# Kernel tuning notes

Measured on AMD Instinct MI355X. Metric: run time of the kernel, lower is better.

## Reference

```python
import jax, jax.numpy as jnp
import numpy as np

N_IN, M_MID = 512, 256
B, H, W = 16, 64, 64

def setup_inputs() -> dict:
    key = jax.random.key(0)
    ks = jax.random.split(key, 7)
    s = 0.05
    return {
        "x": jax.random.normal(ks[0], (B, N_IN, H, W), dtype=jnp.float32),
        "W_state": jax.random.normal(ks[1], (M_MID, N_IN), dtype=jnp.float32) * s,
        "b_state": jax.random.normal(ks[2], (M_MID,), dtype=jnp.float32) * s,
        "W_proj": jax.random.normal(ks[3], (M_MID, N_IN), dtype=jnp.float32) * s,
        "b_proj": jax.random.normal(ks[4], (M_MID,), dtype=jnp.float32) * s,
        "W_extend": jax.random.normal(ks[5], (N_IN, M_MID), dtype=jnp.float32) * s,
        "b_extend": jax.random.normal(ks[6], (N_IN,), dtype=jnp.float32) * s,
    }

def reference(x, W_state, b_state, W_proj, b_proj, W_extend, b_extend):
    n, c, h, w = x.shape
    hw = h * w
    xf = x.reshape(n, c, hw)                                   # [n, C, HW]
    # 1x1 convs are channel GEMMs over flattened spatial dim
    x_state = jnp.einsum('mc,nch->nmh', W_state, xf) + b_state[None, :, None]   # [n, M, HW]
    x_proj = jnp.einsum('mc,nch->nmh', W_proj, xf) + b_proj[None, :, None]      # [n, M, HW]
    # bmm -> scale -> softmax -> bmm (graph reasoning over M x M)
    scores = jnp.einsum('nmh,nkh->nmk', x_state, x_proj) / jnp.sqrt(jnp.float32(hw))
    attn = jax.nn.softmax(scores, axis=2)                      # [n, M, M]
    x_rstate = jnp.einsum('nmk,nkh->nmh', attn, x_proj)        # [n, M, HW]
    # extend back to C channels + residual
    ext = jnp.einsum('cm,nmh->nch', W_extend, x_rstate) + b_extend[None, :, None]
    return x + ext.reshape(n, c, h, w)
```

## Files before the change

### kernel.cpp

```cpp
#include <hip/hip_runtime.h>
#include <hip/hip_bf16.h>
#include <stdint.h>

typedef __bf16 bf16x8_t __attribute__((ext_vector_type(8)));
typedef float  f32x4_t  __attribute__((ext_vector_type(4)));
typedef short  short8_t __attribute__((ext_vector_type(8)));

__device__ __forceinline__ unsigned short f2b(float f) {
    union { float f; unsigned u; } v; v.f = f;
    unsigned u = v.u;
    return (unsigned short)((u + 0x7FFFu + ((u >> 16) & 1u)) >> 16);
}
__device__ __forceinline__ float b2f(unsigned short b) {
    union { unsigned u; float f; } v; v.u = ((unsigned)b) << 16; return v.f;
}

#define AS3(p) ((__attribute__((address_space(3))) void*)(p))
#define AS1(p) ((const __attribute__((address_space(1))) void*)(p))
#define FENCE() asm volatile("" ::: "memory")

#define NB   16
#define CIN  512
#define MMID 256
#define HW   4096
#define KSPLIT 4
#define ASZ  (128 * 64)
#define ASZA3 (256 * 64)
#define ASZB3 (64 * 64)

__device__ __forceinline__ void swz3(int gx, int gy, int& bx, int& by, int& bz) {
    const int nwg = gridDim.x, ord = blockIdx.x, q = nwg >> 3;
    const int s = (ord & 7) * q + (ord >> 3);
    by = s % gy;
    const int rem = s / gy;
    bx = rem % gx;
    bz = rem / gx;
}

__global__ __launch_bounds__(256) void prep_weights(
    const float* __restrict__ Ws, const float* __restrict__ Wp,
    const float* __restrict__ Wef, const float* __restrict__ bs,
    const float* __restrict__ bp,
    unsigned short* __restrict__ Wsp, unsigned short* __restrict__ Wex,
    unsigned short* __restrict__ WpT, float* __restrict__ bsp)
{
    int i = blockIdx.x * 256 + threadIdx.x;
    if (i < MMID * CIN) {
        Wsp[i]              = f2b(Ws[i]);
        Wsp[MMID * CIN + i] = f2b(Wp[i]);
        Wex[i]              = f2b(Wef[i]);
        const int c = i >> 8, k = i & (MMID - 1);
        WpT[i] = f2b(Wp[(size_t)k * CIN + c]);
    }
    if (i < MMID) { bsp[i] = bs[i]; bsp[MMID + i] = bp[i]; }
}

__global__ __launch_bounds__(256) void transpose_convert_x(
    const float* __restrict__ x, unsigned short* __restrict__ xT)
{
    __shared__ unsigned short tile[64][66];
    const int n = blockIdx.z, c0 = blockIdx.y * 64, h0 = blockIdx.x * 64;
    const float* s = x + ((size_t)n * CIN + c0) * HW + h0;
    unsigned short* d = xT + ((size_t)n * HW + h0) * CIN + c0;
    const int t = threadIdx.x;
    {
        const int rr = t >> 4, cc = (t & 15) * 4;
        #pragma unroll
        for (int p = 0; p < 4; ++p) {
            int r = p * 16 + rr;
            float4 v = *(const float4*)(s + (size_t)r * HW + cc);
            tile[r][cc + 0] = f2b(v.x); tile[r][cc + 1] = f2b(v.y);
            tile[r][cc + 2] = f2b(v.z); tile[r][cc + 3] = f2b(v.w);
        }
    }
    __syncthreads();
    {
        const int wr = t >> 3, wc = (t & 7) * 8;
        #pragma unroll
        for (int p = 0; p < 2; ++p) {
            int h = p * 32 + wr;
            unsigned short tmp[8];
            #pragma unroll
            for (int j = 0; j < 8; ++j) tmp[j] = tile[wc + j][h];
            *(short8_t*)(d + (size_t)h * CIN + wc) = *(const short8_t*)tmp;
        }
    }
}

__global__ __launch_bounds__(256) void transpose_bf16_64(
    const unsigned short* __restrict__ src, unsigned short* __restrict__ dst,
    int srs, int drs, long long sbs, long long dbs)
{
    __shared__ unsigned short tile[64][66];
    const int n = blockIdx.z, r0 = blockIdx.y * 64, c0 = blockIdx.x * 64;
    const unsigned short* s = src + (size_t)n * sbs + (size_t)r0 * srs + c0;
    unsigned short* d = dst + (size_t)n * dbs + (size_t)c0 * drs + r0;
    const int t = threadIdx.x;
    const int rr = t >> 3, cc = (t & 7) * 8;
    #pragma unroll
    for (int p = 0; p < 2; ++p) {
        int r = p * 32 + rr;
        short8_t v = *(const short8_t*)(s + (size_t)r * srs + cc);
        #pragma unroll
        for (int j = 0; j < 8; ++j) tile[r][cc + j] = ((const unsigned short*)&v)[j];
    }
    __syncthreads();
    #pragma unroll
    for (int p = 0; p < 2; ++p) {
        int c = p * 32 + rr;
        unsigned short tmp[8];
        #pragma unroll
        for (int j = 0; j < 8; ++j) tmp[j] = tile[cc + j][c];
        *(short8_t*)(d + (size_t)c * drs + cc) = *(const short8_t*)tmp;
    }
}

template <int EPI>
__device__ __forceinline__ void epilogue_repack(
    f32x4_t (&acc)[4][4], unsigned short* smem,
    int m0, int n0, int wave, int lane,
    void* __restrict__ Cout, int ldc, size_t cbase)
{
    float* fbuf = (float*)smem;
    const int t   = wave * 64 + lane;
    const int l15 = lane & 15, l16 = lane >> 4;
    const int wr2 = wave >> 1;
    const int wc  = (wave & 1) * 64;

    #pragma unroll
    for (int p = 0; p < 4; ++p) {
        __syncthreads();
        if (wr2 == (p >> 1)) {
            const int ihalf = p & 1;
            #pragma unroll
            for (int i2 = 0; i2 < 2; ++i2) {
                const int i = ihalf * 2 + i2;
                #pragma unroll
                for (int r = 0; r < 4; ++r) {
                    const int lrow = i2 * 16 + l16 * 4 + r;
                    #pragma unroll
                    for (int j = 0; j < 4; ++j)
                        fbuf[lrow * 132 + wc + j * 16 + l15] = acc[i][j][r];
                }
            }
        }
        __syncthreads();
        #pragma unroll
        for (int it = 0; it < 2; ++it) {
            const int lrow = it * 16 + (t >> 4);
            const int col  = (t & 15) * 8;
            const int row  = m0 + p * 32 + lrow;
            float v[8];
            *(float4*)&v[0] = *(const float4*)&fbuf[lrow * 132 + col];
            *(float4*)&v[4] = *(const float4*)&fbuf[lrow * 132 + col + 4];
            const size_t idx = cbase + (size_t)row * ldc + n0 + col;
            if constexpr (EPI == 1) {
                float* op = (float*)Cout + idx;
                *(float4*)op = *(const float4*)&v[0];
                *(float4*)(op + 4) = *(const float4*)&v[4];
            } else if constexpr (EPI == 4) {
                unsigned short o[8];
                #pragma unroll
                for (int k = 0; k < 8; ++k)
                    o[k] = f2b(v[k] + ((row == n0 + col + k) ? 1.0f : 0.0f));
                *(short8_t*)((unsigned short*)Cout + idx) = *(const short8_t*)o;
            } else {
                unsigned short o[8];
                #pragma unroll
                for (int k = 0; k < 8; ++k) o[k] = f2b(v[k]);
                *(short8_t*)((unsigned short*)Cout + idx) = *(const short8_t*)o;
            }
        }
    }
}

#define GEMM_KLOOP(Ab, Bb, lda, ldb, KBEG, NT)                                          \
    auto stage = [&](int k0, int b) {                                                   \
        unsigned short* Asb = smem + b * 2 * ASZ;                                       \
        unsigned short* Bsb = Asb + ASZ;                                                \
        _Pragma("unroll")                                                               \
        for (int c = 0; c < 4; ++c) {                                                   \
            const int o   = (c * 256 + t) * 16;                                         \
            const int row = o >> 7;                                                     \
            const int ce  = ((o & 127) ^ ((row & 7) << 4)) >> 1;                        \
            __builtin_amdgcn_global_load_lds(                                           \
                AS1(Ab + (size_t)row * lda + k0 + ce), AS3((char*)Asb + o), 16, 0, 0);  \
            __builtin_amdgcn_global_load_lds(                                           \
                AS1(Bb + (size_t)row * ldb + k0 + ce), AS3((char*)Bsb + o), 16, 0, 0);  \
        }                                                                               \
    };                                                                                  \
    stage(KBEG, 0);                                                                     \
    for (int itk = 0; itk < (NT); ++itk) {                                              \
        const int cur = itk & 1;                                                        \
        if (itk + 1 < (NT)) {                                                           \
            stage(KBEG + (itk + 1) * 64, cur ^ 1);                                      \
            asm volatile("s_waitcnt vmcnt(8)" ::: "memory");                            \
        } else {                                                                        \
            asm volatile("s_waitcnt vmcnt(0)" ::: "memory");                            \
        }                                                                               \
        __builtin_amdgcn_s_barrier();                                                   \
        FENCE();                                                                        \
        const char* Asb = (const char*)(smem + cur * 2 * ASZ);                          \
        const char* Bsb = Asb + 2 * ASZ;                                                \
        const int swz = (l15 & 7) << 4;                                                 \
        _Pragma("unroll")                                                               \
        for (int ks = 0; ks < 2; ++ks) {                                                \
            bf16x8_t af[4], bfr[4];                                                     \
            const int cb = (ks * 64 + l16 * 16) ^ swz;                                  \
            _Pragma("unroll")                                                           \
            for (int i = 0; i < 4; ++i) {                                               \
                af[i]  = *(const bf16x8_t*)(Asb + (wr + i * 16 + l15) * 128 + cb);      \
                bfr[i] = *(const bf16x8_t*)(Bsb + (wc + i * 16 + l15) * 128 + cb);      \
            }                                                                           \
            _Pragma("unroll")                                                           \
            for (int i = 0; i < 4; ++i)                                                 \
                _Pragma("unroll")                                                       \
                for (int j = 0; j < 4; ++j)                                             \
                    acc[i][j] = __builtin_amdgcn_mfma_f32_16x16x32_bf16(                \
                        af[i], bfr[j], acc[i][j], 0, 0, 0);                             \
        }                                                                               \
        FENCE();                                                                        \
        __builtin_amdgcn_s_barrier();                                                   \
        FENCE();                                                                        \
    }

template <int EPI>
__global__ __launch_bounds__(256, 2) void gemm_occ2(
    const unsigned short* __restrict__ A, const unsigned short* __restrict__ B,
    long long strideA, long long strideB,
    const float* __restrict__ bias, int bias_bstride,
    void* __restrict__ Cout, int ldc, long long strideC,
    int gx, int gy)
{
    __shared__ unsigned short smem[2 * (ASZA3 + ASZB3)];

    int bx, by, n;  swz3(gx, gy, bx, by, n);
    const int m0 = by * 256;
    const int n0 = bx * 64;

    const unsigned short* Ab = A + (size_t)n * strideA + (size_t)m0 * CIN;
    const unsigned short* Bb = B + (size_t)n * strideB + (size_t)n0 * CIN;

    const int t    = threadIdx.x;
    const int lane = t & 63;
    const int wave = t >> 6;
    const int wr   = wave * 64;
    const int l15  = lane & 15;
    const int l16  = lane >> 4;

    f32x4_t acc[4][4] = {};

    auto stage = [&](int k0, int b) {
        unsigned short* Asb = smem + b * (ASZA3 + ASZB3);
        unsigned short* Bsb = Asb + ASZA3;
        #pragma unroll
        for (int c = 0; c < 8; ++c) {
            const int o   = (c * 256 + t) * 16;
            const int row = o >> 7;
            const int ce  = ((o & 127) ^ ((row & 7) << 4)) >> 1;
            __builtin_amdgcn_global_load_lds(
                AS1(Ab + (size_t)row * CIN + k0 + ce), AS3((char*)Asb + o), 16, 0, 0);
        }
        #pragma unroll
        for (int c = 0; c < 2; ++c) {
            const int o   = (c * 256 + t) * 16;
            const int row = o >> 7;
            const int ce  = ((o & 127) ^ ((row & 7) << 4)) >> 1;
            __builtin_amdgcn_global_load_lds(
                AS1(Bb + (size_t)row * CIN + k0 + ce), AS3((char*)Bsb + o), 16, 0, 0);
        }
    };

    const int NT = CIN / 64;
    stage(0, 0);
    for (int itk = 0; itk < NT; ++itk) {
        const int cur = itk & 1;
        if (itk + 1 < NT) {
            stage((itk + 1) * 64, cur ^ 1);
            asm volatile("s_waitcnt vmcnt(10)" ::: "memory");
        } else {
            asm volatile("s_waitcnt vmcnt(0)" ::: "memory");
        }
        __builtin_amdgcn_s_barrier();
        FENCE();
        const char* Asb = (const char*)(smem + cur * (ASZA3 + ASZB3));
        const char* Bsb = Asb + 2 * ASZA3;
        const int swz = (l15 & 7) << 4;
        #pragma unroll
        for (int ks = 0; ks < 2; ++ks) {
            const int cb = (ks * 64 + l16 * 16) ^ swz;
            bf16x8_t af[4], bfr[4];
            #pragma unroll
            for (int i = 0; i < 4; ++i)
                af[i] = *(const bf16x8_t*)(Asb + (wr + i * 16 + l15) * 128 + cb);
            #pragma unroll
            for (int j = 0; j < 4; ++j)
                bfr[j] = *(const bf16x8_t*)(Bsb + (j * 16 + l15) * 128 + cb);
            #pragma unroll
            for (int i = 0; i < 4; ++i)
                #pragma unroll
                for (int j = 0; j < 4; ++j)
                    acc[i][j] = __builtin_amdgcn_mfma_f32_16x16x32_bf16(
                        af[i], bfr[j], acc[i][j], 0, 0, 0);
        }
        FENCE();
        __builtin_amdgcn_s_barrier();
        FENCE();
    }

    float* fbuf = (float*)smem;
    const size_t cbase = (size_t)n * strideC;
    const float* beff = bias + (size_t)n * bias_bstride;
    #pragma unroll
    for (int p = 0; p < 8; ++p) {
        __syncthreads();
        if (wave == (p >> 1)) {
            #pragma unroll
            for (int i2 = 0; i2 < 2; ++i2) {
                const int i = (p & 1) * 2 + i2;
                #pragma unroll
                for (int r = 0; r < 4; ++r) {
                    const int lrow = i2 * 16 + l16 * 4 + r;
                    #pragma unroll
                    for (int j = 0; j < 4; ++j)
                        fbuf[lrow * 68 + j * 16 + l15] = acc[i][j][r];
                }
            }
        }
        __syncthreads();
        const int lrow = t >> 3;
        const int col  = (t & 7) * 8;
        const int row  = m0 + p * 32 + lrow;
        float v[8];
        *(float4*)&v[0] = *(const float4*)&fbuf[lrow * 68 + col];
        *(float4*)&v[4] = *(const float4*)&fbuf[lrow * 68 + col + 4];
        const float badd = beff[row];
        const size_t idx = cbase + (size_t)row * ldc + n0 + col;
        if constexpr (EPI == 1) {
            float o[8];
            #pragma unroll
            for (int k = 0; k < 8; ++k) o[k] = v[k] + badd;
            float* op = (float*)Cout + idx;
            *(float4*)op = *(const float4*)&o[0];
            *(float4*)(op + 4) = *(const float4*)&o[4];
        } else {
            unsigned short o[8];
            #pragma unroll
            for (int k = 0; k < 8; ++k) o[k] = f2b(v[k] + badd);
            *(short8_t*)((unsigned short*)Cout + idx) = *(const short8_t*)o;
        }
    }
}

__global__ __launch_bounds__(256) void gemm_scores(
    const unsigned short* __restrict__ Ysp, float* __restrict__ scoresP)
{
    __shared__ unsigned short smem[4 * ASZ];

    int bx, by, z;  swz3(MMID / 128, MMID / 128, bx, by, z);
    const int n  = z >> 2;
    const int kc = z & 3;
    const int m0 = by * 128;
    const int n0 = bx * 128;

    const unsigned short* Ab = Ysp + (size_t)n * CIN * HW + (size_t)m0 * HW;
    const unsigned short* Bb = Ysp + (size_t)n * CIN * HW + (size_t)(MMID + n0) * HW;

    const int t    = threadIdx.x;
    const int lane = t & 63;
    const int wave = t >> 6;
    const int wr   = (wave >> 1) * 64;
    const int wc   = (wave & 1) * 64;
    const int l15  = lane & 15;
    const int l16  = lane >> 4;

    f32x4_t acc[4][4] = {};
    const int kbeg = kc * (HW / KSPLIT);
    GEMM_KLOOP(Ab, Bb, HW, HW, kbeg, (HW / KSPLIT) / 64)

    float* outp = scoresP + (size_t)(kc * NB + n) * MMID * MMID;
    epilogue_repack<1>(acc, smem, m0, n0, wave, lane, outp, MMID, 0);
}

__global__ __launch_bounds__(256) void softmax_rows(
    const float* __restrict__ scoresP, unsigned short* __restrict__ attn)
{
    const int wave = threadIdx.x >> 6;
    const int l    = threadIdx.x & 63;
    const size_t row = (size_t)blockIdx.x * 4 + wave;
    const size_t pstride = (size_t)NB * MMID * MMID;
    float4 v = {0.f, 0.f, 0.f, 0.f};
    #pragma unroll
    for (int p = 0; p < KSPLIT; ++p) {
        float4 u = *(const float4*)(scoresP + p * pstride + row * MMID + l * 4);
        v.x += u.x; v.y += u.y; v.z += u.z; v.w += u.w;
    }
    float mx = fmaxf(fmaxf(v.x, v.y), fmaxf(v.z, v.w));
    #pragma unroll
    for (int off = 32; off; off >>= 1) mx = fmaxf(mx, __shfl_xor(mx, off));
    const float sc = 0.015625f;
    float e0 = __expf((v.x - mx) * sc), e1 = __expf((v.y - mx) * sc);
    float e2 = __expf((v.z - mx) * sc), e3 = __expf((v.w - mx) * sc);
    float sum = e0 + e1 + e2 + e3;
    #pragma unroll
    for (int off = 32; off; off >>= 1) sum += __shfl_xor(sum, off);
    const float inv = 1.0f / sum;
    unsigned short o[4] = { f2b(e0 * inv), f2b(e1 * inv), f2b(e2 * inv), f2b(e3 * inv) };
    *(uint64_t*)(attn + row * MMID + l * 4) = *(const uint64_t*)o;
}

__global__ __launch_bounds__(256) void compute_vec(
    const unsigned short* __restrict__ G, const float* __restrict__ bsp,
    const float* __restrict__ be, float* __restrict__ vec)
{
    const int n = blockIdx.x >> 1;
    const int c = ((blockIdx.x & 1) << 8) + threadIdx.x;
    const unsigned short* g = G + ((size_t)n * CIN + c) * MMID;
    float s = 0.f;
    for (int k = 0; k < MMID; k += 8) {
        short8_t v = *(const short8_t*)(g + k);
        #pragma unroll
        for (int j = 0; j < 8; ++j)
            s += b2f((unsigned short)v[j]) * bsp[MMID + k + j];
    }
    vec[n * CIN + c] = be[c] + s;
}

template <int EPI>
__global__ __launch_bounds__(256) void gemm_nt(
    const unsigned short* __restrict__ A, const unsigned short* __restrict__ B,
    int lda, int ldb, int K,
    long long strideA, long long strideB,
    void* __restrict__ Cout, int ldc, long long strideC,
    int gx, int gy)
{
    __shared__ unsigned short smem[4 * ASZ];

    int bx, by, n;  swz3(gx, gy, bx, by, n);
    const int m0 = by * 128;
    const int n0 = bx * 128;

    const unsigned short* Ab = A + (size_t)n * strideA + (size_t)m0 * lda;
    const unsigned short* Bb = B + (size_t)n * strideB + (size_t)n0 * ldb;

    const int t    = threadIdx.x;
    const int lane = t & 63;
    const int wave = t >> 6;
    const int wr   = (wave >> 1) * 64;
    const int wc   = (wave & 1) * 64;
    const int l15  = lane & 15;
    const int l16  = lane >> 4;

    f32x4_t acc[4][4] = {};
    GEMM_KLOOP(Ab, Bb, lda, ldb, 0, K / 64)

    epilogue_repack<EPI>(acc, smem, m0, n0, wave, lane,
                         Cout, ldc, (size_t)n * strideC);
}

extern "C" void kernel_launch(void* const* d_in, const int* in_sizes, int n_in,
                              void* d_out, int out_size, void* d_ws, size_t ws_size,
                              hipStream_t stream)
{
    const float* x   = (const float*)d_in[0];
    const float* Ws  = (const float*)d_in[1];
    const float* bs  = (const float*)d_in[2];
    const float* Wp  = (const float*)d_in[3];
    const float* bp  = (const float*)d_in[4];
    const float* Wef = (const float*)d_in[5];
    const float* be  = (const float*)d_in[6];
    float* out = (float*)d_out;

    unsigned short* xT   = (unsigned short*)d_ws;
    unsigned short* Ysp  = xT   + (size_t)NB * HW * CIN;
    unsigned short* Wsp  = Ysp  + (size_t)NB * CIN * HW;
    unsigned short* Wex  = Wsp  + (size_t)CIN * CIN;
    unsigned short* WpT  = Wex  + (size_t)CIN * MMID;
    unsigned short* attn = WpT  + (size_t)CIN * MMID;
    unsigned short* attnT= attn + (size_t)NB * MMID * MMID;
    unsigned short* G    = attnT+ (size_t)NB * MMID * MMID;
    unsigned short* Meff = G    + (size_t)NB * CIN * MMID;
    float* scoresP = (float*)(Meff + (size_t)NB * CIN * CIN);
    float* bsp = scoresP + (size_t)KSPLIT * NB * MMID * MMID;
    float* vec = bsp + CIN;

    prep_weights<<<512, 256, 0, stream>>>(Ws, Wp, Wef, bs, bp, Wsp, Wex, WpT, bsp);

    transpose_convert_x<<<dim3(HW / 64, CIN / 64, NB), 256, 0, stream>>>(x, xT);

    gemm_occ2<0><<<(CIN / 256) * (HW / 64) * NB, 256, 0, stream>>>(
        Wsp, xT, 0LL, (long long)HW * CIN,
        bsp, 0, Ysp, HW, (long long)CIN * HW,
        HW / 64, CIN / 256);

    gemm_scores<<<(MMID / 128) * (MMID / 128) * NB * KSPLIT, 256, 0, stream>>>(
        Ysp, scoresP);

    softmax_rows<<<NB * MMID / 4, 256, 0, stream>>>(scoresP, attn);

    transpose_bf16_64<<<dim3(MMID / 64, MMID / 64, NB), 256, 0, stream>>>(
        attn, attnT, MMID, MMID, (long long)MMID * MMID, (long long)MMID * MMID);

    gemm_nt<2><<<(MMID / 128) * (CIN / 128) * NB, 256, 0, stream>>>(
        Wex, attnT, MMID, MMID, MMID,
        0LL, (long long)MMID * MMID,
        G, MMID, (long long)CIN * MMID,
        MMID / 128, CIN / 128);

    compute_vec<<<NB * 2, 256, 0, stream>>>(G, bsp, be, vec);

    gemm_nt<4><<<(CIN / 128) * (CIN / 128) * NB, 256, 0, stream>>>(
        G, WpT, MMID, MMID, MMID,
        (long long)CIN * MMID, 0LL,
        Meff, CIN, (long long)CIN * CIN,
        CIN / 128, CIN / 128);

    gemm_occ2<1><<<(CIN / 256) * (HW / 64) * NB, 256, 0, stream>>>(
        Meff, xT, (long long)CIN * CIN, (long long)HW * CIN,
        vec, CIN, out, HW, (long long)CIN * HW,
        HW / 64, CIN / 256);
}
```

Before: 197.4 us.

## Replace occupancy-2 GEMM with 256x256-tile 8-wave eight-phase pipelined GEMM

The two big channel GEMMs (Wsp·x and Meff·x) move from a 256x64 tile with 4 waves and 2 blocks per CU to a 256x256 tile with 8 waves and one block per CU. The K loop is split into half-K-tile phases that interleave LDS fragment reads, async global-to-LDS loads and MFMA bursts raised with s_setprio. The LDS layout also gets a new XOR swizzle. The aim is more operand reuse per loaded byte and better overlap of memory traffic with compute, at the cost of lower occupancy, higher register pressure (128 accumulator floats per lane) and a more rigid synchronisation schedule.

```diff
diff --git a/kernel.cpp b/kernel.cpp
--- a/kernel.cpp
+++ b/kernel.cpp
@@ -25,8 +25,7 @@
 #define HW   4096
 #define KSPLIT 4
 #define ASZ  (128 * 64)
-#define ASZA3 (256 * 64)
-#define ASZB3 (64 * 64)
+#define PH_BUFB 65536
 
 __device__ __forceinline__ void swz3(int gx, int gy, int& bx, int& by, int& bz) {
     const int nwg = gridDim.x, ord = blockIdx.x, q = nwg >> 3;
@@ -225,18 +224,18 @@
     }
 
 template <int EPI>
-__global__ __launch_bounds__(256, 2) void gemm_occ2(
+__global__ __launch_bounds__(512, 1) void gemm_8ph(
     const unsigned short* __restrict__ A, const unsigned short* __restrict__ B,
     long long strideA, long long strideB,
     const float* __restrict__ bias, int bias_bstride,
     void* __restrict__ Cout, int ldc, long long strideC,
     int gx, int gy)
 {
-    __shared__ unsigned short smem[2 * (ASZA3 + ASZB3)];
+    __shared__ __attribute__((aligned(16))) char smem[2 * PH_BUFB];
 
     int bx, by, n;  swz3(gx, gy, bx, by, n);
     const int m0 = by * 256;
-    const int n0 = bx * 64;
+    const int n0 = bx * 256;
 
     const unsigned short* Ab = A + (size_t)n * strideA + (size_t)m0 * CIN;
     const unsigned short* Bb = B + (size_t)n * strideB + (size_t)n0 * CIN;
@@ -244,69 +243,96 @@
     const int t    = threadIdx.x;
     const int lane = t & 63;
     const int wave = t >> 6;
-    const int wr   = wave * 64;
+    const int wr2  = wave >> 2;
+    const int wc4  = wave & 3;
     const int l15  = lane & 15;
     const int l16  = lane >> 4;
 
-    f32x4_t acc[4][4] = {};
-
-    auto stage = [&](int k0, int b) {
-        unsigned short* Asb = smem + b * (ASZA3 + ASZB3);
-        unsigned short* Bsb = Asb + ASZA3;
-        #pragma unroll
-        for (int c = 0; c < 8; ++c) {
-            const int o   = (c * 256 + t) * 16;
-            const int row = o >> 7;
-            const int ce  = ((o & 127) ^ ((row & 7) << 4)) >> 1;
+    auto stage_half = [&](const unsigned short* base, int kt, int kh, char* dst) {
+        #pragma unroll
+        for (int c = 0; c < 2; ++c) {
+            const int ci = c * 512 + t;
+            const int r  = ci >> 2;
+            const int ssrc = (ci & 3) ^ ((r >> 1) & 3);
             __builtin_amdgcn_global_load_lds(
-                AS1(Ab + (size_t)row * CIN + k0 + ce), AS3((char*)Asb + o), 16, 0, 0);
-        }
-        #pragma unroll
-        for (int c = 0; c < 2; ++c) {
-            const int o   = (c * 256 + t) * 16;
-            const int row = o >> 7;
-            const int ce  = ((o & 127) ^ ((row & 7) << 4)) >> 1;
-            __builtin_amdgcn_global_load_lds(
-                AS1(Bb + (size_t)row * CIN + k0 + ce), AS3((char*)Bsb + o), 16, 0, 0);
+                AS1(base + (size_t)r * CIN + kt * 64 + kh * 32 + ssrc * 8),
+                AS3(dst + ci * 16), 16, 0, 0);
         }
     };
 
-    const int NT = CIN / 64;
-    stage(0, 0);
-    for (int itk = 0; itk < NT; ++itk) {
-        const int cur = itk & 1;
-        if (itk + 1 < NT) {
-            stage((itk + 1) * 64, cur ^ 1);
-            asm volatile("s_waitcnt vmcnt(10)" ::: "memory");
-        } else {
-            asm volatile("s_waitcnt vmcnt(0)" ::: "memory");
-        }
-        __builtin_amdgcn_s_barrier();
-        FENCE();
-        const char* Asb = (const char*)(smem + cur * (ASZA3 + ASZB3));
-        const char* Bsb = Asb + 2 * ASZA3;
-        const int swz = (l15 & 7) << 4;
-        #pragma unroll
-        for (int ks = 0; ks < 2; ++ks) {
-            const int cb = (ks * 64 + l16 * 16) ^ swz;
-            bf16x8_t af[4], bfr[4];
-            #pragma unroll
-            for (int i = 0; i < 4; ++i)
-                af[i] = *(const bf16x8_t*)(Asb + (wr + i * 16 + l15) * 128 + cb);
-            #pragma unroll
-            for (int j = 0; j < 4; ++j)
-                bfr[j] = *(const bf16x8_t*)(Bsb + (j * 16 + l15) * 128 + cb);
-            #pragma unroll
-            for (int i = 0; i < 4; ++i)
-                #pragma unroll
-                for (int j = 0; j < 4; ++j)
-                    acc[i][j] = __builtin_amdgcn_mfma_f32_16x16x32_bf16(
-                        af[i], bfr[j], acc[i][j], 0, 0, 0);
-        }
-        FENCE();
-        __builtin_amdgcn_s_barrier();
-        FENCE();
-    }
+    f32x4_t acc[8][4] = {};
+    bf16x8_t af4[4], bfr4[4];
+
+    auto read_af = [&](int ibase, int ks, const char* buf) {
+        #pragma unroll
+        for (int i = 0; i < 4; ++i) {
+            const int row = wr2 * 128 + (ibase + i) * 16 + l15;
+            af4[i] = *(const bf16x8_t*)(buf + ks * 16384 + row * 64
+                         + ((l16 ^ ((row >> 1) & 3)) << 4));
+        }
+    };
+    auto read_bfr = [&](int ks, const char* buf) {
+        #pragma unroll
+        for (int j = 0; j < 4; ++j) {
+            const int row = wc4 * 64 + j * 16 + l15;
+            bfr4[j] = *(const bf16x8_t*)(buf + 32768 + ks * 16384 + row * 64
+                         + ((l16 ^ ((row >> 1) & 3)) << 4));
+        }
+    };
+
+    #define PH_SYNC() do { asm volatile("s_waitcnt vmcnt(8)" ::: "memory"); \
+        __builtin_amdgcn_s_barrier(); FENCE(); } while (0)
+    #define PH_END() do { FENCE(); __builtin_amdgcn_s_barrier(); FENCE(); } while (0)
+    #define MFMA16(IB) do { __builtin_amdgcn_s_setprio(1); \
+        _Pragma("unroll") for (int i = 0; i < 4; ++i) \
+            _Pragma("unroll") for (int j = 0; j < 4; ++j) \
+                acc[(IB) + i][j] = __builtin_amdgcn_mfma_f32_16x16x32_bf16( \
+                    af4[i], bfr4[j], acc[(IB) + i][j], 0, 0, 0); \
+        __builtin_amdgcn_s_setprio(0); } while (0)
+
+    char* buf0 = smem;
+    char* buf1 = smem + PH_BUFB;
+
+    stage_half(Ab, 0, 0, buf0 + 0);
+    stage_half(Bb, 0, 0, buf0 + 32768);
+    stage_half(Ab, 0, 1, buf0 + 16384);
+    stage_half(Bb, 0, 1, buf0 + 49152);
+    stage_half(Ab, 1, 0, buf1 + 0);
+    stage_half(Bb, 1, 0, buf1 + 32768);
+    asm volatile("s_waitcnt vmcnt(8)" ::: "memory");
+    __builtin_amdgcn_s_barrier();
+    FENCE();
+
+    for (int g = 0; g < 4; ++g) {
+        const int t2 = 2 * g + 2, t3 = 2 * g + 3;
+        read_af(0, 0, buf0); read_bfr(0, buf0);
+        stage_half(Ab, 2 * g + 1, 1, buf1 + 16384);
+        PH_SYNC(); MFMA16(0); PH_END();
+        read_af(4, 0, buf0);
+        stage_half(Bb, 2 * g + 1, 1, buf1 + 49152);
+        PH_SYNC(); MFMA16(4); PH_END();
+        read_af(0, 1, buf0); read_bfr(1, buf0);
+        if (t2 < 8) stage_half(Ab, t2, 0, buf0 + 0);
+        PH_SYNC(); MFMA16(0); PH_END();
+        read_af(4, 1, buf0);
+        if (t2 < 8) stage_half(Bb, t2, 0, buf0 + 32768);
+        PH_SYNC(); MFMA16(4); PH_END();
+        read_af(0, 0, buf1); read_bfr(0, buf1);
+        if (t2 < 8) stage_half(Ab, t2, 1, buf0 + 16384);
+        PH_SYNC(); MFMA16(0); PH_END();
+        read_af(4, 0, buf1);
+        if (t2 < 8) stage_half(Bb, t2, 1, buf0 + 49152);
+        PH_SYNC(); MFMA16(4); PH_END();
+        read_af(0, 1, buf1); read_bfr(1, buf1);
+        if (t3 < 8) stage_half(Ab, t3, 0, buf1 + 0);
+        PH_SYNC(); MFMA16(0); PH_END();
+        read_af(4, 1, buf1);
+        if (t3 < 8) stage_half(Bb, t3, 0, buf1 + 32768);
+        PH_SYNC(); MFMA16(4); PH_END();
+    }
+    #undef PH_SYNC
+    #undef PH_END
+    #undef MFMA16
 
     float* fbuf = (float*)smem;
     const size_t cbase = (size_t)n * strideC;
@@ -314,40 +340,43 @@
     #pragma unroll
     for (int p = 0; p < 8; ++p) {
         __syncthreads();
-        if (wave == (p >> 1)) {
+        if (wr2 == (p >> 2)) {
             #pragma unroll
             for (int i2 = 0; i2 < 2; ++i2) {
-                const int i = (p & 1) * 2 + i2;
+                const int i = (p & 3) * 2 + i2;
                 #pragma unroll
                 for (int r = 0; r < 4; ++r) {
                     const int lrow = i2 * 16 + l16 * 4 + r;
                     #pragma unroll
                     for (int j = 0; j < 4; ++j)
-                        fbuf[lrow * 68 + j * 16 + l15] = acc[i][j][r];
+                        fbuf[lrow * 264 + wc4 * 64 + j * 16 + l15] = acc[i][j][r];
                 }
             }
         }
         __syncthreads();
-        const int lrow = t >> 3;
-        const int col  = (t & 7) * 8;
-        const int row  = m0 + p * 32 + lrow;
-        float v[8];
-        *(float4*)&v[0] = *(const float4*)&fbuf[lrow * 68 + col];
-        *(float4*)&v[4] = *(const float4*)&fbuf[lrow * 68 + col + 4];
-        const float badd = beff[row];
-        const size_t idx = cbase + (size_t)row * ldc + n0 + col;
-        if constexpr (EPI == 1) {
-            float o[8];
-            #pragma unroll
-            for (int k = 0; k < 8; ++k) o[k] = v[k] + badd;
-            float* op = (float*)Cout + idx;
-            *(float4*)op = *(const float4*)&o[0];
-            *(float4*)(op + 4) = *(const float4*)&o[4];
-        } else {
-            unsigned short o[8];
-            #pragma unroll
-            for (int k = 0; k < 8; ++k) o[k] = f2b(v[k] + badd);
-            *(short8_t*)((unsigned short*)Cout + idx) = *(const short8_t*)o;
+        #pragma unroll
+        for (int it = 0; it < 2; ++it) {
+            const int lrow = it * 16 + (t >> 5);
+            const int col  = (t & 31) * 8;
+            const int row  = m0 + p * 32 + lrow;
+            float v[8];
+            *(float4*)&v[0] = *(const float4*)&fbuf[lrow * 264 + col];
+            *(float4*)&v[4] = *(const float4*)&fbuf[lrow * 264 + col + 4];
+            const float badd = beff[row];
+            const size_t idx = cbase + (size_t)row * ldc + n0 + col;
+            if constexpr (EPI == 1) {
+                float o[8];
+                #pragma unroll
+                for (int k = 0; k < 8; ++k) o[k] = v[k] + badd;
+                float* op = (float*)Cout + idx;
+                *(float4*)op = *(const float4*)&o[0];
+                *(float4*)(op + 4) = *(const float4*)&o[4];
+            } else {
+                unsigned short o[8];
+                #pragma unroll
+                for (int k = 0; k < 8; ++k) o[k] = f2b(v[k] + badd);
+                *(short8_t*)((unsigned short*)Cout + idx) = *(const short8_t*)o;
+            }
         }
     }
 }
@@ -488,10 +517,10 @@
 
     transpose_convert_x<<<dim3(HW / 64, CIN / 64, NB), 256, 0, stream>>>(x, xT);
 
-    gemm_occ2<0><<<(CIN / 256) * (HW / 64) * NB, 256, 0, stream>>>(
+    gemm_8ph<0><<<(HW / 256) * (CIN / 256) * NB, 512, 0, stream>>>(
         Wsp, xT, 0LL, (long long)HW * CIN,
         bsp, 0, Ysp, HW, (long long)CIN * HW,
-        HW / 64, CIN / 256);
+        HW / 256, CIN / 256);
 
     gemm_scores<<<(MMID / 128) * (MMID / 128) * NB * KSPLIT, 256, 0, stream>>>(
         Ysp, scoresP);
@@ -515,8 +544,8 @@
         Meff, CIN, (long long)CIN * CIN,
         CIN / 128, CIN / 128);
 
-    gemm_occ2<1><<<(CIN / 256) * (HW / 64) * NB, 256, 0, stream>>>(
+    gemm_8ph<1><<<(HW / 256) * (CIN / 256) * NB, 512, 0, stream>>>(
         Meff, xT, (long long)CIN * CIN, (long long)HW * CIN,
         vec, CIN, out, HW, (long long)CIN * HW,
-        HW / 64, CIN / 256);
-}
+        HW / 256, CIN / 256);
+}
```

New measurement: 199.9 us. About the same (+1.3%).

## Widen big GEMM tiles to 256x128 with 8 waves and K=32 stages

Applied to the files above, without the earlier changes.

Restructures the two large x-side GEMMs to use a 256x128 output tile computed by 512 threads (8 waves in a 4x2 grid), with a K step of 32 instead of 64 and a 4-way LDS swizzle to match. Each staged B tile is now reused across twice as many output columns, which cuts global traffic per FLOP and halves the grid. The change also raises MFMA scheduling priority with s_setprio and widens the epilogue staging buffer to 128 columns. In exchange the pipeline runs twice as many k-iterations, each with a barrier, and per-block LDS and register pressure rises, which may limit occupancy.

```diff
diff --git a/kernel.cpp b/kernel.cpp
--- a/kernel.cpp
+++ b/kernel.cpp
@@ -25,8 +25,8 @@
 #define HW   4096
 #define KSPLIT 4
 #define ASZ  (128 * 64)
-#define ASZA3 (256 * 64)
-#define ASZB3 (64 * 64)
+#define A4E  (256 * 32)
+#define B4E  (128 * 32)
 
 __device__ __forceinline__ void swz3(int gx, int gy, int& bx, int& by, int& bz) {
     const int nwg = gridDim.x, ord = blockIdx.x, q = nwg >> 3;
@@ -225,18 +225,18 @@
     }
 
 template <int EPI>
-__global__ __launch_bounds__(256, 2) void gemm_occ2(
+__global__ __launch_bounds__(512, 3) void gemm_bn128(
     const unsigned short* __restrict__ A, const unsigned short* __restrict__ B,
     long long strideA, long long strideB,
     const float* __restrict__ bias, int bias_bstride,
     void* __restrict__ Cout, int ldc, long long strideC,
     int gx, int gy)
 {
-    __shared__ unsigned short smem[2 * (ASZA3 + ASZB3)];
+    __shared__ unsigned short smem[2 * (A4E + B4E)];
 
     int bx, by, n;  swz3(gx, gy, bx, by, n);
     const int m0 = by * 256;
-    const int n0 = bx * 64;
+    const int n0 = bx * 128;
 
     const unsigned short* Ab = A + (size_t)n * strideA + (size_t)m0 * CIN;
     const unsigned short* Bb = B + (size_t)n * strideB + (size_t)n0 * CIN;
@@ -244,65 +244,66 @@
     const int t    = threadIdx.x;
     const int lane = t & 63;
     const int wave = t >> 6;
-    const int wr   = wave * 64;
+    const int wr   = (wave >> 1) * 64;
+    const int wc   = (wave & 1) * 64;
     const int l15  = lane & 15;
     const int l16  = lane >> 4;
 
     f32x4_t acc[4][4] = {};
 
     auto stage = [&](int k0, int b) {
-        unsigned short* Asb = smem + b * (ASZA3 + ASZB3);
-        unsigned short* Bsb = Asb + ASZA3;
-        #pragma unroll
-        for (int c = 0; c < 8; ++c) {
-            const int o   = (c * 256 + t) * 16;
-            const int row = o >> 7;
-            const int ce  = ((o & 127) ^ ((row & 7) << 4)) >> 1;
+        unsigned short* Asb = smem + b * (A4E + B4E);
+        unsigned short* Bsb = Asb + A4E;
+        #pragma unroll
+        for (int c = 0; c < 2; ++c) {
+            const int ci  = c * 512 + t;
+            const int row = ci >> 2;
+            const int ce  = (((ci & 3) * 16) ^ ((row & 3) << 4)) >> 1;
             __builtin_amdgcn_global_load_lds(
-                AS1(Ab + (size_t)row * CIN + k0 + ce), AS3((char*)Asb + o), 16, 0, 0);
-        }
-        #pragma unroll
-        for (int c = 0; c < 2; ++c) {
-            const int o   = (c * 256 + t) * 16;
-            const int row = o >> 7;
-            const int ce  = ((o & 127) ^ ((row & 7) << 4)) >> 1;
+                AS1(Ab + (size_t)row * CIN + k0 + ce), AS3((char*)Asb + ci * 16), 16, 0, 0);
+        }
+        {
+            const int ci  = t;
+            const int row = ci >> 2;
+            const int ce  = (((ci & 3) * 16) ^ ((row & 3) << 4)) >> 1;
             __builtin_amdgcn_global_load_lds(
-                AS1(Bb + (size_t)row * CIN + k0 + ce), AS3((char*)Bsb + o), 16, 0, 0);
+                AS1(Bb + (size_t)row * CIN + k0 + ce), AS3((char*)Bsb + ci * 16), 16, 0, 0);
         }
     };
 
-    const int NT = CIN / 64;
+    const int NT = CIN / 32;
     stage(0, 0);
     for (int itk = 0; itk < NT; ++itk) {
         const int cur = itk & 1;
         if (itk + 1 < NT) {
-            stage((itk + 1) * 64, cur ^ 1);
-            asm volatile("s_waitcnt vmcnt(10)" ::: "memory");
+            stage((itk + 1) * 32, cur ^ 1);
+            asm volatile("s_waitcnt vmcnt(3)" ::: "memory");
         } else {
             asm volatile("s_waitcnt vmcnt(0)" ::: "memory");
         }
         __builtin_amdgcn_s_barrier();
         FENCE();
-        const char* Asb = (const char*)(smem + cur * (ASZA3 + ASZB3));
-        const char* Bsb = Asb + 2 * ASZA3;
-        const int swz = (l15 & 7) << 4;
-        #pragma unroll
-        for (int ks = 0; ks < 2; ++ks) {
-            const int cb = (ks * 64 + l16 * 16) ^ swz;
-            bf16x8_t af[4], bfr[4];
-            #pragma unroll
-            for (int i = 0; i < 4; ++i)
-                af[i] = *(const bf16x8_t*)(Asb + (wr + i * 16 + l15) * 128 + cb);
+        const char* Asb = (const char*)(smem + cur * (A4E + B4E));
+        const char* Bsb = Asb + 2 * A4E;
+        bf16x8_t af[4], bfr[4];
+        #pragma unroll
+        for (int i = 0; i < 4; ++i) {
+            const int row = wr + i * 16 + l15;
+            af[i] = *(const bf16x8_t*)(Asb + row * 64 + ((l16 * 16) ^ ((row & 3) << 4)));
+        }
+        #pragma unroll
+        for (int j = 0; j < 4; ++j) {
+            const int row = wc + j * 16 + l15;
+            bfr[j] = *(const bf16x8_t*)(Bsb + row * 64 + ((l16 * 16) ^ ((row & 3) << 4)));
+        }
+        __builtin_amdgcn_s_setprio(1);
+        #pragma unroll
+        for (int i = 0; i < 4; ++i)
             #pragma unroll
             for (int j = 0; j < 4; ++j)
-                bfr[j] = *(const bf16x8_t*)(Bsb + (j * 16 + l15) * 128 + cb);
-            #pragma unroll
-            for (int i = 0; i < 4; ++i)
-                #pragma unroll
-                for (int j = 0; j < 4; ++j)
-                    acc[i][j] = __builtin_amdgcn_mfma_f32_16x16x32_bf16(
-                        af[i], bfr[j], acc[i][j], 0, 0, 0);
-        }
+                acc[i][j] = __builtin_amdgcn_mfma_f32_16x16x32_bf16(
+                    af[i], bfr[j], acc[i][j], 0, 0, 0);
+        __builtin_amdgcn_s_setprio(0);
         FENCE();
         __builtin_amdgcn_s_barrier();
         FENCE();
@@ -314,7 +315,7 @@
     #pragma unroll
     for (int p = 0; p < 8; ++p) {
         __syncthreads();
-        if (wave == (p >> 1)) {
+        if ((wave >> 1) == (p >> 1)) {
             #pragma unroll
             for (int i2 = 0; i2 < 2; ++i2) {
                 const int i = (p & 1) * 2 + i2;
@@ -323,17 +324,17 @@
                     const int lrow = i2 * 16 + l16 * 4 + r;
                     #pragma unroll
                     for (int j = 0; j < 4; ++j)
-                        fbuf[lrow * 68 + j * 16 + l15] = acc[i][j][r];
+                        fbuf[lrow * 132 + wc + j * 16 + l15] = acc[i][j][r];
                 }
             }
         }
         __syncthreads();
-        const int lrow = t >> 3;
-        const int col  = (t & 7) * 8;
+        const int lrow = t >> 4;
+        const int col  = (t & 15) * 8;
         const int row  = m0 + p * 32 + lrow;
         float v[8];
-        *(float4*)&v[0] = *(const float4*)&fbuf[lrow * 68 + col];
-        *(float4*)&v[4] = *(const float4*)&fbuf[lrow * 68 + col + 4];
+        *(float4*)&v[0] = *(const float4*)&fbuf[lrow * 132 + col];
+        *(float4*)&v[4] = *(const float4*)&fbuf[lrow * 132 + col + 4];
         const float badd = beff[row];
         const size_t idx = cbase + (size_t)row * ldc + n0 + col;
         if constexpr (EPI == 1) {
@@ -488,10 +489,10 @@
 
     transpose_convert_x<<<dim3(HW / 64, CIN / 64, NB), 256, 0, stream>>>(x, xT);
 
-    gemm_occ2<0><<<(CIN / 256) * (HW / 64) * NB, 256, 0, stream>>>(
+    gemm_bn128<0><<<(CIN / 256) * (HW / 128) * NB, 512, 0, stream>>>(
         Wsp, xT, 0LL, (long long)HW * CIN,
         bsp, 0, Ysp, HW, (long long)CIN * HW,
-        HW / 64, CIN / 256);
+        HW / 128, CIN / 256);
 
     gemm_scores<<<(MMID / 128) * (MMID / 128) * NB * KSPLIT, 256, 0, stream>>>(
         Ysp, scoresP);
@@ -515,8 +516,8 @@
         Meff, CIN, (long long)CIN * CIN,
         CIN / 128, CIN / 128);
 
-    gemm_occ2<1><<<(CIN / 256) * (HW / 64) * NB, 256, 0, stream>>>(
+    gemm_bn128<1><<<(CIN / 256) * (HW / 128) * NB, 512, 0, stream>>>(
         Meff, xT, (long long)CIN * CIN, (long long)HW * CIN,
         vec, CIN, out, HW, (long long)CIN * HW,
-        HW / 64, CIN / 256);
-}
+        HW / 128, CIN / 256);
+}
```

Result: slower. 220.8 us (+11.9%).
